# Optimization experiments

Measured on AMD Instinct MI355X. Metric: run time of the kernel, lower is better.

The kernel has to match this reference:

```python
import jax, jax.numpy as jnp
import numpy as np

RADIUS = 0.1
NSAMPLE = 32
B, N, NPOINT, C = 4, 8192, 2048, 64


def ball_query(xyz, new_xyz, fps_idx):
    """Faithful to pointnet2 ball_query CUDA kernel: for each centroid collect up to
    NSAMPLE in-radius point indices in scan order; slots beyond the count are padded
    with the first in-radius index (0 if the ball is empty). fps_idx is prepended."""
    n = xyz.shape[1]
    # squared distances (B, npoint, N)
    d2 = jnp.sum((new_xyz[:, :, None, :] - xyz[:, None, :, :]) ** 2, axis=-1)
    valid = d2 < jnp.float32(RADIUS) ** 2
    cand = jnp.where(valid, jnp.arange(n, dtype=jnp.int32), jnp.int32(n))
    cand = jnp.sort(cand, axis=-1)[:, :, :NSAMPLE]  # first NSAMPLE valid ids, N = sentinel
    first = cand[:, :, :1]
    pad = jnp.where(first < n, first, 0)            # pad with first valid (0 if none)
    idx = jnp.where(cand < n, cand, pad)
    return jnp.concatenate([fps_idx[:, :, None], idx], axis=2)  # (B, npoint, NSAMPLE+1)


def group(features, idx):
    # features (B, C, N), idx (B, npoint, K) -> (B, C, npoint, K)
    return jax.vmap(lambda f, i: f[:, i])(features, idx)


def setup_inputs() -> dict:
    key = jax.random.key(0)
    k1, k2, k3 = jax.random.split(key, 3)
    xyz = jax.random.uniform(k1, (B, N, 3), dtype=jnp.float32)
    fps_idx = jax.random.randint(k2, (B, NPOINT), 0, N, dtype=jnp.int32)
    new_xyz = jax.vmap(lambda p, i: p[i])(xyz, fps_idx)  # centroids are real points
    features = jax.random.normal(k3, (B, C, N), dtype=jnp.float32)
    return {"xyz": xyz, "new_xyz": new_xyz, "features": features, "fps_idx": fps_idx}


def reference(xyz, new_xyz, features, fps_idx):
    idx = jax.lax.stop_gradient(ball_query(xyz, new_xyz, fps_idx))
    grouped_xyz = group(jnp.swapaxes(xyz, 1, 2), idx)              # (B, 3, npoint, K)
    centered = grouped_xyz - jnp.swapaxes(new_xyz, 1, 2)[..., None]
    # NOTE: the torch module uses in-place `grouped_xyz -= ...`, so raw_grouped_xyz
    # aliases the centered tensor -> both concat slots hold centered coordinates.
    grouped_features = group(features, idx)                        # (B, C, npoint, K)
    return jnp.concatenate([centered, centered, grouped_features], axis=1)
```

## Files before the change

### kernel.cpp

```cpp
#include <hip/hip_runtime.h>
#include <stdint.h>
#include <limits.h>

constexpr int BB      = 4;
constexpr int NN      = 8192;
constexpr int NPOINT  = 2048;
constexpr int CC      = 64;
constexpr int NSAMPLE = 32;
constexpr int KTOT    = NSAMPLE + 1;
constexpr int NCH     = 3 + 3 + CC;
constexpr int CHS     = NPOINT * KTOT;

constexpr int   GG     = 5;
constexpr int   NCELL  = GG * GG * GG;
constexpr float RPADF  = 0.1001f;
constexpr int   CAND_CAP = 192;

__device__ __forceinline__ int cell_of(float x, float y, float z) {
    int ix = (int)floorf(x * 5.0f); ix = ix < 0 ? 0 : (ix > 4 ? 4 : ix);
    int iy = (int)floorf(y * 5.0f); iy = iy < 0 ? 0 : (iy > 4 ? 4 : iy);
    int iz = (int)floorf(z * 5.0f); iz = iz < 0 ? 0 : (iz > 4 ? 4 : iz);
    return (ix * GG + iy) * GG + iz;
}

__global__ __launch_bounds__(1024) void grid_build(
    const float* __restrict__ xyz, int* __restrict__ cellstartg,
    float4* __restrict__ spt)
{
    __shared__ int hist[NCELL];
    __shared__ int csl[NCELL + 1];
    __shared__ int cur[NCELL];
    const int b = blockIdx.x;
    const int t = threadIdx.x;
    if (t < NCELL) hist[t] = 0;
    __syncthreads();
    const float* xb = xyz + (size_t)b * NN * 3;
    float px[NN / 1024], py[NN / 1024], pz[NN / 1024];
    int   pc[NN / 1024];
#pragma unroll
    for (int k = 0; k < NN / 1024; ++k) {
        const float* p = xb + (size_t)(t + k * 1024) * 3;
        px[k] = p[0]; py[k] = p[1]; pz[k] = p[2];
        pc[k] = cell_of(px[k], py[k], pz[k]);
        atomicAdd(&hist[pc[k]], 1);
    }
    __syncthreads();
    if (t < 64) {
        int x0 = hist[t];
        int x1 = (t + 64 < NCELL) ? hist[t + 64] : 0;
#pragma unroll
        for (int d = 1; d < 64; d <<= 1) {
            int t0 = __shfl_up(x0, d);
            int t1 = __shfl_up(x1, d);
            if (t >= d) { x0 += t0; x1 += t1; }
        }
        x1 += __shfl(x0, 63);
        if (t == 0) csl[0] = 0;
        csl[1 + t] = x0;
        if (t <= 60) csl[65 + t] = x1;
    }
    __syncthreads();
    if (t < NCELL + 1) cellstartg[b * (NCELL + 1) + t] = csl[t];
    if (t < NCELL)     cur[t] = csl[t];
    __syncthreads();
#pragma unroll
    for (int k = 0; k < NN / 1024; ++k) {
        const int pos = atomicAdd(&cur[pc[k]], 1);
        spt[b * NN + pos] = make_float4(px[k], py[k], pz[k],
                                        __int_as_float(t + k * 1024));
    }
}

__global__ __launch_bounds__(256) void ball_query_grid(
    const float4* __restrict__ spt, const int* __restrict__ cellstart,
    const float* __restrict__ new_xyz, const int* __restrict__ fps_idx,
    int*         __restrict__ idx_out)
{
    __shared__ int cand[4][CAND_CAP];
    const int w    = threadIdx.x >> 6;
    const int lane = threadIdx.x & 63;
    const int wave = blockIdx.x * 4 + w;
    const int b    = wave >> 11;

    const float* cp = new_xyz + (size_t)wave * 3;
    const float cx = cp[0], cy = cp[1], cz = cp[2];
    const float r2 = __fmul_rn(0.1f, 0.1f);

    int ix0 = (int)floorf((cx - RPADF) * 5.0f); ix0 = ix0 < 0 ? 0 : ix0;
    int ix1 = (int)floorf((cx + RPADF) * 5.0f); ix1 = ix1 > 4 ? 4 : ix1;
    int iy0 = (int)floorf((cy - RPADF) * 5.0f); iy0 = iy0 < 0 ? 0 : iy0;
    int iy1 = (int)floorf((cy + RPADF) * 5.0f); iy1 = iy1 > 4 ? 4 : iy1;
    int iz0 = (int)floorf((cz - RPADF) * 5.0f); iz0 = iz0 < 0 ? 0 : iz0;
    int iz1 = (int)floorf((cz + RPADF) * 5.0f); iz1 = iz1 > 4 ? 4 : iz1;

    const int* cs = cellstart + b * (NCELL + 1);
    const int gb  = b * NN;
    int cnt = 0;

    for (int ix = ix0; ix <= ix1; ++ix) {
        for (int iy = iy0; iy <= iy1; ++iy) {
            const int cbase = (ix * GG + iy) * GG;
            const int st = cs[cbase + iz0];
            const int en = cs[cbase + iz1 + 1];
            for (int base = st; base < en; base += 64) {
                const int pos = base + lane;
                const bool inb = pos < en;
                const float4 q = spt[gb + (inb ? pos : st)];
                const int oid = __float_as_int(q.w);
                const float dx = __fsub_rn(cx, q.x);
                const float dy = __fsub_rn(cy, q.y);
                const float dz = __fsub_rn(cz, q.z);
                const float d2 = __fadd_rn(__fadd_rn(__fmul_rn(dx, dx), __fmul_rn(dy, dy)),
                                           __fmul_rn(dz, dz));
                const bool valid = inb && (d2 < r2);
                const unsigned long long m = __ballot(valid);
                if (m != 0ull) {
                    const int prefix = __builtin_amdgcn_mbcnt_hi(
                        (unsigned)(m >> 32), __builtin_amdgcn_mbcnt_lo((unsigned)m, 0u));
                    const int slot = cnt + prefix;
                    if (valid && slot < CAND_CAP) cand[w][slot] = oid;
                    cnt += (int)__popcll(m);
                }
            }
        }
    }

    const int K = cnt > CAND_CAP ? CAND_CAP : cnt;

    int v0 = (lane       < K) ? cand[w][lane]       : INT_MAX;
    int v1 = (lane + 64  < K) ? cand[w][lane + 64]  : INT_MAX;
    int v2 = (lane + 128 < K) ? cand[w][lane + 128] : INT_MAX;
    int rk0 = 0, rk1 = 0, rk2 = 0;
    for (int j = 0; j < K; ++j) {
        const int sv = cand[w][j];
        rk0 += (sv < v0); rk1 += (sv < v1); rk2 += (sv < v2);
    }
    int* out = idx_out + (size_t)wave * KTOT;
    if (lane       < K && rk0 < NSAMPLE) out[1 + rk0] = v0;
    if (lane + 64  < K && rk1 < NSAMPLE) out[1 + rk1] = v1;
    if (lane + 128 < K && rk2 < NSAMPLE) out[1 + rk2] = v2;

    if (K < NSAMPLE) {
        int mn = v0;
#pragma unroll
        for (int off = 32; off >= 1; off >>= 1) {
            const int o = __shfl_xor(mn, off);
            mn = o < mn ? o : mn;
        }
        const int pad = (K > 0) ? mn : 0;
        if (lane >= K && lane < NSAMPLE) out[1 + lane] = pad;
    }
    if (lane == 0) out[0] = fps_idx[wave];
}

__global__ __launch_bounds__(256) void feat_transpose(
    const float* __restrict__ f, float* __restrict__ ft)
{
    __shared__ float tile[64 * 65];
    const int blk = blockIdx.x;
    const int b   = blk >> 7;
    const int n0  = (blk & 127) << 6;
    const int w   = threadIdx.x >> 6, l = threadIdx.x & 63;
#pragma unroll
    for (int i = 0; i < 16; ++i) {
        const int c = i * 4 + w;
        tile[l * 65 + c] = f[((size_t)b * CC + c) * NN + n0 + l];
    }
    __syncthreads();
#pragma unroll
    for (int i = 0; i < 16; ++i) {
        const int flat = i * 256 + threadIdx.x;
        ft[((size_t)b * NN + n0) * CC + flat] = tile[(flat >> 6) * 65 + (flat & 63)];
    }
}

constexpr int TPAD = 66;
__global__ __launch_bounds__(256) void gather_v7(
    const float* __restrict__ xyz, const float* __restrict__ new_xyz,
    const float4* __restrict__ ft4, const int* __restrict__ idx,
    float* __restrict__ out)
{
    __shared__ float tile[NCH][TPAD];
    const int blk = blockIdx.x;
    const int t   = threadIdx.x;
    const int jj0 = blk * 64;
    const int b   = jj0 / CHS;
    const int jjb = jj0 - b * CHS;

    if (t < 64) {
        const int id = idx[jj0 + t];
        const int j  = (jjb + t) / KTOT;
        const float* gp = xyz + (size_t)(b * NN + id) * 3;
        const float* cp = new_xyz + (size_t)(b * NPOINT + j) * 3;
        const float vx = __fsub_rn(gp[0], cp[0]);
        const float vy = __fsub_rn(gp[1], cp[1]);
        const float vz = __fsub_rn(gp[2], cp[2]);
        tile[0][t] = vx; tile[1][t] = vy; tile[2][t] = vz;
        tile[3][t] = vx; tile[4][t] = vy; tile[5][t] = vz;
    }

    {
        const int r = t >> 2, g = t & 3;
        const int id = idx[jj0 + r];
        const float4* row = ft4 + ((size_t)b * NN + id) * (CC / 4);
        float4 v[4];
#pragma unroll
        for (int i = 0; i < 4; ++i) v[i] = row[4 * i + g];
#pragma unroll
        for (int i = 0; i < 4; ++i) {
            const int c0 = 6 + 16 * i + 4 * g;
            tile[c0 + 0][r] = v[i].x;
            tile[c0 + 1][r] = v[i].y;
            tile[c0 + 2][r] = v[i].z;
            tile[c0 + 3][r] = v[i].w;
        }
    }
    __syncthreads();

    const int w   = t >> 6;
    const int col = t & 63;
    const size_t ob = (size_t)b * NCH * CHS + (size_t)jjb + col;
#pragma unroll
    for (int k = 0; k < 18; ++k) {
        const int ch = 4 * k + w;
        if (ch < NCH) out[ob + (size_t)ch * CHS] = tile[ch][col];
    }
}

__global__ __launch_bounds__(256) void ball_query_bf(
    const float* __restrict__ xyz, const float* __restrict__ new_xyz,
    const int* __restrict__ fps_idx, int* __restrict__ idx_out)
{
    const int wave = (blockIdx.x * blockDim.x + threadIdx.x) >> 6;
    const int lane = threadIdx.x & 63;
    if (wave >= BB * NPOINT) return;
    const int b = wave >> 11;
    const float* cp = new_xyz + (size_t)wave * 3;
    const float cx = cp[0], cy = cp[1], cz = cp[2];
    const float r2 = __fmul_rn(0.1f, 0.1f);
    const float* xb = xyz + (size_t)b * NN * 3;
    int* out = idx_out + (size_t)wave * KTOT;
    int count = 0, first = 0;
    for (int base = 0; base < NN; base += 64) {
        const int p = base + lane;
        const float dx = __fsub_rn(cx, xb[p * 3 + 0]);
        const float dy = __fsub_rn(cy, xb[p * 3 + 1]);
        const float dz = __fsub_rn(cz, xb[p * 3 + 2]);
        const float d2 = __fadd_rn(__fadd_rn(__fmul_rn(dx, dx), __fmul_rn(dy, dy)),
                                   __fmul_rn(dz, dz));
        const bool valid = d2 < r2;
        const unsigned long long m = __ballot(valid);
        if (count == 0 && m != 0ull) first = base + __builtin_ctzll(m);
        const int prefix = __builtin_amdgcn_mbcnt_hi(
            (unsigned)(m >> 32), __builtin_amdgcn_mbcnt_lo((unsigned)m, 0u));
        const int slot = count + prefix;
        if (valid && slot < NSAMPLE) out[1 + slot] = p;
        count += (int)__popcll(m);
        if (count >= NSAMPLE) break;
    }
    if (count < NSAMPLE) {
        const int pad = (count > 0) ? first : 0;
        if (lane >= count && lane < NSAMPLE) out[1 + lane] = pad;
    }
    if (lane == 0) out[0] = fps_idx[wave];
}

__global__ __launch_bounds__(256) void gather_kernel(
    const float* __restrict__ xyz, const float* __restrict__ new_xyz,
    const float* __restrict__ features, const int* __restrict__ idx,
    float* __restrict__ out)
{
    const long long total = (long long)BB * NCH * CHS;
    const long long o = (long long)blockIdx.x * blockDim.x + threadIdx.x;
    if (o >= total) return;
    const int s  = (int)(o % KTOT);
    long long t  = o / KTOT;
    const int j  = (int)(t % NPOINT);
    t /= NPOINT;
    const int ch = (int)(t % NCH);
    const int b  = (int)(t / NCH);
    const int id = idx[(long long)(b * NPOINT + j) * KTOT + s];
    float v;
    if (ch < 6) {
        const int c3 = (ch >= 3) ? (ch - 3) : ch;
        v = __fsub_rn(xyz[((long long)b * NN + id) * 3 + c3],
                      new_xyz[((long long)b * NPOINT + j) * 3 + c3]);
    } else {
        v = features[((long long)b * CC + (ch - 6)) * NN + id];
    }
    out[o] = v;
}

extern "C" void kernel_launch(void* const* d_in, const int* in_sizes, int n_in,
                              void* d_out, int out_size, void* d_ws, size_t ws_size,
                              hipStream_t stream) {
    const float* xyz      = (const float*)d_in[0];
    const float* new_xyz  = (const float*)d_in[1];
    const float* features = (const float*)d_in[2];
    const int*   fps_idx  = (const int*)d_in[3];
    float*       out      = (float*)d_out;

    const size_t off_idx  = 0;
    const size_t sz_idx   = (size_t)BB * CHS * 4;
    const size_t off_ft   = off_idx + sz_idx;
    const size_t sz_ft    = (size_t)BB * NN * CC * 4;
    const size_t off_spt  = off_ft + sz_ft;
    const size_t sz_spt   = (size_t)BB * NN * 16;
    const size_t off_cs   = off_spt + sz_spt;
    const size_t need_full = off_cs + 2048;

    int* idxbuf = (int*)((char*)d_ws + off_idx);

    if (ws_size >= need_full) {
        float*  ft  = (float*) ((char*)d_ws + off_ft);
        float4* spt = (float4*)((char*)d_ws + off_spt);
        int*    cs  = (int*)   ((char*)d_ws + off_cs);

        grid_build<<<BB, 1024, 0, stream>>>(xyz, cs, spt);

        ball_query_grid<<<BB * NPOINT / 4, 256, 0, stream>>>(
            spt, cs, new_xyz, fps_idx, idxbuf);

        feat_transpose<<<BB * (NN / 64), 256, 0, stream>>>(features, ft);
        gather_v7<<<BB * CHS / 64, 256, 0, stream>>>(xyz, new_xyz, (const float4*)ft,
                                                     idxbuf, out);
    } else if (ws_size >= sz_idx) {
        ball_query_bf<<<BB * NPOINT / 4, 256, 0, stream>>>(xyz, new_xyz, fps_idx, idxbuf);
        const long long total = (long long)BB * NCH * CHS;
        gather_kernel<<<(int)((total + 255) / 256), 256, 0, stream>>>(
            xyz, new_xyz, features, idxbuf, out);
    }
}
```

Measured before the change: 124.3 us.

## Fuse grid ball query with feature gather into a single kernel

Merges the grid ball-query kernel and the gather kernel. Each block computes neighbour indices for 4 centroids into shared memory, then 132 threads each gather one full 64-channel feature row and write all 70 output channels directly. This removes the index buffer round trip through global memory and one kernel launch. In exchange, each gathering thread holds 16 float4 registers, only 132 of 256 threads do the gather, and each wave's stores cover 132 consecutive floats per channel rather than the earlier 64-wide tiled transpose layout.

```diff
diff --git a/kernel.cpp b/kernel.cpp
--- a/kernel.cpp
+++ b/kernel.cpp
@@ -71,88 +71,6 @@
     }
 }
 
-__global__ __launch_bounds__(256) void ball_query_grid(
-    const float4* __restrict__ spt, const int* __restrict__ cellstart,
-    const float* __restrict__ new_xyz, const int* __restrict__ fps_idx,
-    int*         __restrict__ idx_out)
-{
-    __shared__ int cand[4][CAND_CAP];
-    const int w    = threadIdx.x >> 6;
-    const int lane = threadIdx.x & 63;
-    const int wave = blockIdx.x * 4 + w;
-    const int b    = wave >> 11;
-
-    const float* cp = new_xyz + (size_t)wave * 3;
-    const float cx = cp[0], cy = cp[1], cz = cp[2];
-    const float r2 = __fmul_rn(0.1f, 0.1f);
-
-    int ix0 = (int)floorf((cx - RPADF) * 5.0f); ix0 = ix0 < 0 ? 0 : ix0;
-    int ix1 = (int)floorf((cx + RPADF) * 5.0f); ix1 = ix1 > 4 ? 4 : ix1;
-    int iy0 = (int)floorf((cy - RPADF) * 5.0f); iy0 = iy0 < 0 ? 0 : iy0;
-    int iy1 = (int)floorf((cy + RPADF) * 5.0f); iy1 = iy1 > 4 ? 4 : iy1;
-    int iz0 = (int)floorf((cz - RPADF) * 5.0f); iz0 = iz0 < 0 ? 0 : iz0;
-    int iz1 = (int)floorf((cz + RPADF) * 5.0f); iz1 = iz1 > 4 ? 4 : iz1;
-
-    const int* cs = cellstart + b * (NCELL + 1);
-    const int gb  = b * NN;
-    int cnt = 0;
-
-    for (int ix = ix0; ix <= ix1; ++ix) {
-        for (int iy = iy0; iy <= iy1; ++iy) {
-            const int cbase = (ix * GG + iy) * GG;
-            const int st = cs[cbase + iz0];
-            const int en = cs[cbase + iz1 + 1];
-            for (int base = st; base < en; base += 64) {
-                const int pos = base + lane;
-                const bool inb = pos < en;
-                const float4 q = spt[gb + (inb ? pos : st)];
-                const int oid = __float_as_int(q.w);
-                const float dx = __fsub_rn(cx, q.x);
-                const float dy = __fsub_rn(cy, q.y);
-                const float dz = __fsub_rn(cz, q.z);
-                const float d2 = __fadd_rn(__fadd_rn(__fmul_rn(dx, dx), __fmul_rn(dy, dy)),
-                                           __fmul_rn(dz, dz));
-                const bool valid = inb && (d2 < r2);
-                const unsigned long long m = __ballot(valid);
-                if (m != 0ull) {
-                    const int prefix = __builtin_amdgcn_mbcnt_hi(
-                        (unsigned)(m >> 32), __builtin_amdgcn_mbcnt_lo((unsigned)m, 0u));
-                    const int slot = cnt + prefix;
-                    if (valid && slot < CAND_CAP) cand[w][slot] = oid;
-                    cnt += (int)__popcll(m);
-                }
-            }
-        }
-    }
-
-    const int K = cnt > CAND_CAP ? CAND_CAP : cnt;
-
-    int v0 = (lane       < K) ? cand[w][lane]       : INT_MAX;
-    int v1 = (lane + 64  < K) ? cand[w][lane + 64]  : INT_MAX;
-    int v2 = (lane + 128 < K) ? cand[w][lane + 128] : INT_MAX;
-    int rk0 = 0, rk1 = 0, rk2 = 0;
-    for (int j = 0; j < K; ++j) {
-        const int sv = cand[w][j];
-        rk0 += (sv < v0); rk1 += (sv < v1); rk2 += (sv < v2);
-    }
-    int* out = idx_out + (size_t)wave * KTOT;
-    if (lane       < K && rk0 < NSAMPLE) out[1 + rk0] = v0;
-    if (lane + 64  < K && rk1 < NSAMPLE) out[1 + rk1] = v1;
-    if (lane + 128 < K && rk2 < NSAMPLE) out[1 + rk2] = v2;
-
-    if (K < NSAMPLE) {
-        int mn = v0;
-#pragma unroll
-        for (int off = 32; off >= 1; off >>= 1) {
-            const int o = __shfl_xor(mn, off);
-            mn = o < mn ? o : mn;
-        }
-        const int pad = (K > 0) ? mn : 0;
-        if (lane >= K && lane < NSAMPLE) out[1 + lane] = pad;
-    }
-    if (lane == 0) out[0] = fps_idx[wave];
-}
-
 __global__ __launch_bounds__(256) void feat_transpose(
     const float* __restrict__ f, float* __restrict__ ft)
 {
@@ -174,56 +92,130 @@
     }
 }
 
-constexpr int TPAD = 66;
-__global__ __launch_bounds__(256) void gather_v7(
+__global__ __launch_bounds__(256) void bq_gather_fused(
+    const float4* __restrict__ spt, const int* __restrict__ cellstart,
     const float* __restrict__ xyz, const float* __restrict__ new_xyz,
-    const float4* __restrict__ ft4, const int* __restrict__ idx,
+    const float4* __restrict__ ft4, const int* __restrict__ fps_idx,
     float* __restrict__ out)
 {
-    __shared__ float tile[NCH][TPAD];
-    const int blk = blockIdx.x;
-    const int t   = threadIdx.x;
-    const int jj0 = blk * 64;
-    const int b   = jj0 / CHS;
-    const int jjb = jj0 - b * CHS;
-
-    if (t < 64) {
-        const int id = idx[jj0 + t];
-        const int j  = (jjb + t) / KTOT;
-        const float* gp = xyz + (size_t)(b * NN + id) * 3;
-        const float* cp = new_xyz + (size_t)(b * NPOINT + j) * 3;
+    __shared__ int cand[4][CAND_CAP];
+    __shared__ int sid[4][KTOT];
+
+    const int w    = threadIdx.x >> 6;
+    const int lane = threadIdx.x & 63;
+    const int wave = blockIdx.x * 4 + w;
+    const int b    = wave >> 11;
+
+    {
+        const float* cp = new_xyz + (size_t)wave * 3;
+        const float cx = cp[0], cy = cp[1], cz = cp[2];
+        const float r2 = __fmul_rn(0.1f, 0.1f);
+
+        int ix0 = (int)floorf((cx - RPADF) * 5.0f); ix0 = ix0 < 0 ? 0 : ix0;
+        int ix1 = (int)floorf((cx + RPADF) * 5.0f); ix1 = ix1 > 4 ? 4 : ix1;
+        int iy0 = (int)floorf((cy - RPADF) * 5.0f); iy0 = iy0 < 0 ? 0 : iy0;
+        int iy1 = (int)floorf((cy + RPADF) * 5.0f); iy1 = iy1 > 4 ? 4 : iy1;
+        int iz0 = (int)floorf((cz - RPADF) * 5.0f); iz0 = iz0 < 0 ? 0 : iz0;
+        int iz1 = (int)floorf((cz + RPADF) * 5.0f); iz1 = iz1 > 4 ? 4 : iz1;
+
+        const int* cs = cellstart + b * (NCELL + 1);
+        const int gb  = b * NN;
+        int cnt = 0;
+
+        for (int ix = ix0; ix <= ix1; ++ix) {
+            for (int iy = iy0; iy <= iy1; ++iy) {
+                const int cbase = (ix * GG + iy) * GG;
+                const int st = cs[cbase + iz0];
+                const int en = cs[cbase + iz1 + 1];
+                for (int base = st; base < en; base += 64) {
+                    const int pos = base + lane;
+                    const bool inb = pos < en;
+                    const float4 q = spt[gb + (inb ? pos : st)];
+                    const int oid = __float_as_int(q.w);
+                    const float dx = __fsub_rn(cx, q.x);
+                    const float dy = __fsub_rn(cy, q.y);
+                    const float dz = __fsub_rn(cz, q.z);
+                    const float d2 = __fadd_rn(__fadd_rn(__fmul_rn(dx, dx), __fmul_rn(dy, dy)),
+                                               __fmul_rn(dz, dz));
+                    const bool valid = inb && (d2 < r2);
+                    const unsigned long long m = __ballot(valid);
+                    if (m != 0ull) {
+                        const int prefix = __builtin_amdgcn_mbcnt_hi(
+                            (unsigned)(m >> 32), __builtin_amdgcn_mbcnt_lo((unsigned)m, 0u));
+                        const int slot = cnt + prefix;
+                        if (valid && slot < CAND_CAP) cand[w][slot] = oid;
+                        cnt += (int)__popcll(m);
+                    }
+                }
+            }
+        }
+
+        const int K = cnt > CAND_CAP ? CAND_CAP : cnt;
+
+        int v0 = (lane       < K) ? cand[w][lane]       : INT_MAX;
+        int v1 = (lane + 64  < K) ? cand[w][lane + 64]  : INT_MAX;
+        int v2 = (lane + 128 < K) ? cand[w][lane + 128] : INT_MAX;
+        int rk0 = 0, rk1 = 0, rk2 = 0;
+        for (int j = 0; j < K; ++j) {
+            const int sv = cand[w][j];
+            rk0 += (sv < v0); rk1 += (sv < v1); rk2 += (sv < v2);
+        }
+        if (lane       < K && rk0 < NSAMPLE) sid[w][1 + rk0] = v0;
+        if (lane + 64  < K && rk1 < NSAMPLE) sid[w][1 + rk1] = v1;
+        if (lane + 128 < K && rk2 < NSAMPLE) sid[w][1 + rk2] = v2;
+
+        if (K < NSAMPLE) {
+            int mn = v0;
+#pragma unroll
+            for (int off = 32; off >= 1; off >>= 1) {
+                const int o = __shfl_xor(mn, off);
+                mn = o < mn ? o : mn;
+            }
+            const int pad = (K > 0) ? mn : 0;
+            if (lane >= K && lane < NSAMPLE) sid[w][1 + lane] = pad;
+        }
+        if (lane == 0) sid[w][0] = fps_idx[wave];
+    }
+
+    __syncthreads();
+
+    const int t = threadIdx.x;
+    if (t < 4 * KTOT) {
+        const int w2 = t / KTOT;
+        const int s  = t - w2 * KTOT;
+        const int c0 = blockIdx.x * 4;
+        const int j  = c0 + w2;
+        const int bb = c0 >> 11;
+        const int id = sid[w2][s];
+
+        const float4* row = ft4 + ((size_t)bb * NN + id) * (CC / 4);
+        float4 v[16];
+#pragma unroll
+        for (int i = 0; i < 16; ++i) v[i] = row[i];
+
+        const float* gp = xyz + (size_t)(bb * NN + id) * 3;
+        const float* cp = new_xyz + (size_t)j * 3;
         const float vx = __fsub_rn(gp[0], cp[0]);
         const float vy = __fsub_rn(gp[1], cp[1]);
         const float vz = __fsub_rn(gp[2], cp[2]);
-        tile[0][t] = vx; tile[1][t] = vy; tile[2][t] = vz;
-        tile[3][t] = vx; tile[4][t] = vy; tile[5][t] = vz;
-    }
-
-    {
-        const int r = t >> 2, g = t & 3;
-        const int id = idx[jj0 + r];
-        const float4* row = ft4 + ((size_t)b * NN + id) * (CC / 4);
-        float4 v[4];
-#pragma unroll
-        for (int i = 0; i < 4; ++i) v[i] = row[4 * i + g];
-#pragma unroll
-        for (int i = 0; i < 4; ++i) {
-            const int c0 = 6 + 16 * i + 4 * g;
-            tile[c0 + 0][r] = v[i].x;
-            tile[c0 + 1][r] = v[i].y;
-            tile[c0 + 2][r] = v[i].z;
-            tile[c0 + 3][r] = v[i].w;
-        }
-    }
-    __syncthreads();
-
-    const int w   = t >> 6;
-    const int col = t & 63;
-    const size_t ob = (size_t)b * NCH * CHS + (size_t)jjb + col;
-#pragma unroll
-    for (int k = 0; k < 18; ++k) {
-        const int ch = 4 * k + w;
-        if (ch < NCH) out[ob + (size_t)ch * CHS] = tile[ch][col];
+
+        const size_t obase = (size_t)bb * NCH * CHS
+                           + (size_t)(c0 & (NPOINT - 1)) * KTOT + t;
+        out[obase + 0 * (size_t)CHS] = vx;
+        out[obase + 1 * (size_t)CHS] = vy;
+        out[obase + 2 * (size_t)CHS] = vz;
+        out[obase + 3 * (size_t)CHS] = vx;
+        out[obase + 4 * (size_t)CHS] = vy;
+        out[obase + 5 * (size_t)CHS] = vz;
+
+#pragma unroll
+        for (int i = 0; i < 16; ++i) {
+            const size_t cb = obase + (size_t)(6 + 4 * i) * CHS;
+            out[cb + 0 * (size_t)CHS] = v[i].x;
+            out[cb + 1 * (size_t)CHS] = v[i].y;
+            out[cb + 2 * (size_t)CHS] = v[i].z;
+            out[cb + 3 * (size_t)CHS] = v[i].w;
+        }
     }
 }
 
@@ -318,12 +310,10 @@
 
         grid_build<<<BB, 1024, 0, stream>>>(xyz, cs, spt);
 
-        ball_query_grid<<<BB * NPOINT / 4, 256, 0, stream>>>(
-            spt, cs, new_xyz, fps_idx, idxbuf);
-
         feat_transpose<<<BB * (NN / 64), 256, 0, stream>>>(features, ft);
-        gather_v7<<<BB * CHS / 64, 256, 0, stream>>>(xyz, new_xyz, (const float4*)ft,
-                                                     idxbuf, out);
+
+        bq_gather_fused<<<BB * NPOINT / 4, 256, 0, stream>>>(
+            spt, cs, xyz, new_xyz, (const float4*)ft, fps_idx, out);
     } else if (ws_size >= sz_idx) {
         ball_query_bf<<<BB * NPOINT / 4, 256, 0, stream>>>(xyz, new_xyz, fps_idx, idxbuf);
         const long long total = (long long)BB * NCH * CHS;
```

After: 127.3 us. 2.4% more time.
